# Kernel tuning notes

Measured on AMD Instinct MI355X. Metric: run time of the kernel, lower is better.

The kernel has to match this reference:

```python
import jax, jax.numpy as jnp
import numpy as np

N_EMBD = 768
N_HEAD = 12
HEAD_DIM = N_EMBD // N_HEAD


def setup_inputs() -> dict:
    key = jax.random.key(0)
    ks = jax.random.split(key, 9)
    s = 0.02
    return {
        "x": jax.random.normal(ks[0], (2, 4096, N_EMBD), dtype=jnp.float32),
        "Wq": jax.random.normal(ks[1], (N_EMBD, N_EMBD), dtype=jnp.float32) * s,
        "bq": jnp.zeros((N_EMBD,), dtype=jnp.float32),
        "Wk": jax.random.normal(ks[2], (N_EMBD, N_EMBD), dtype=jnp.float32) * s,
        "bk": jnp.zeros((N_EMBD,), dtype=jnp.float32),
        "Wv": jax.random.normal(ks[3], (N_EMBD, N_EMBD), dtype=jnp.float32) * s,
        "bv": jnp.zeros((N_EMBD,), dtype=jnp.float32),
        "Wo": jax.random.normal(ks[4], (N_EMBD, N_EMBD), dtype=jnp.float32) * s,
        "bo": jnp.zeros((N_EMBD,), dtype=jnp.float32),
    }


def reference(x, Wq, bq, Wk, bk, Wv, bv, Wo, bo):
    B, T, C = x.shape
    H, D = N_HEAD, HEAD_DIM
    # torch Linear: y = x @ W.T + b
    q = (x @ Wq.T + bq).reshape(B, T, H, D).transpose(0, 2, 1, 3)  # [B,H,T,D]
    k = (x @ Wk.T + bk).reshape(B, T, H, D).transpose(0, 2, 1, 3)
    v = (x @ Wv.T + bv).reshape(B, T, H, D).transpose(0, 2, 1, 3)
    scale = 1.0 / jnp.sqrt(jnp.float32(D))
    att = jnp.einsum("bhqd,bhkd->bhqk", q, k) * scale  # [B,H,T,T]
    causal = jnp.tril(jnp.ones((T, T), dtype=bool))
    att = jnp.where(causal[None, None], att, -jnp.inf)
    att = jax.nn.softmax(att, axis=-1)
    y = jnp.einsum("bhqk,bhkd->bhqd", att, v)
    y = y.transpose(0, 2, 1, 3).reshape(B, T, C)
    return y @ Wo.T + bo
```

## Files before the change

kernel.cpp:

```cpp
#include <hip/hip_runtime.h>

typedef __bf16 bf16_t;
typedef __bf16 bf16x4 __attribute__((ext_vector_type(4)));
typedef __bf16 bf16x8 __attribute__((ext_vector_type(8)));
typedef float  f32x4  __attribute__((ext_vector_type(4)));
typedef float  f32x16 __attribute__((ext_vector_type(16)));
typedef unsigned int u32;

#define MFMA16(a, b, c) __builtin_amdgcn_mfma_f32_16x16x32_bf16((a), (b), (c), 0, 0, 0)
#define MFMA32(a, b, c) __builtin_amdgcn_mfma_f32_32x32x16_bf16((a), (b), (c), 0, 0, 0)

__device__ __forceinline__ void gld_lds16(const bf16_t* g, bf16_t* l) {
  __builtin_amdgcn_global_load_lds((__attribute__((address_space(1))) void*)g,
                                   (__attribute__((address_space(3))) void*)l, 16, 0, 0);
}
__device__ __forceinline__ u32 cvt_pk_bf16(float lo, float hi) {
  u32 r;
  asm("v_cvt_pk_bf16_f32 %0, %1, %2" : "=v"(r) : "v"(lo), "v"(hi));
  return r;
}

__global__ void cast_f32_bf16(const float* __restrict__ s, bf16_t* __restrict__ d, int n) {
  int i = (blockIdx.x * blockDim.x + threadIdx.x) * 4;
  if (i >= n) return;
  float4 v = *(const float4*)(s + i);
  bf16x4 o;
  o[0] = (bf16_t)v.x; o[1] = (bf16_t)v.y; o[2] = (bf16_t)v.z; o[3] = (bf16_t)v.w;
  *(bf16x4*)(d + i) = o;
}

__global__ void concat_bias(const float* __restrict__ a, const float* __restrict__ b,
                            const float* __restrict__ c, float* __restrict__ d) {
  int i = blockIdx.x * blockDim.x + threadIdx.x;
  if (i >= 2304) return;
  d[i] = i < 768 ? a[i] : (i < 1536 ? b[i - 768] : c[i - 1536]);
}

__global__ __launch_bounds__(256) void gemm_qkv(
    const bf16_t* __restrict__ A, const bf16_t* __restrict__ B,
    const float* __restrict__ bias,
    bf16_t* __restrict__ qb, bf16_t* __restrict__ kb2, bf16_t* __restrict__ vtb) {
  __shared__ __align__(16) bf16_t As[128 * 64];
  __shared__ __align__(16) bf16_t Bs[128 * 64];
  const int K = 768;
  const int bm = blockIdx.x, bn = blockIdx.y;
  const int tid = threadIdx.x;
  const int w = tid >> 6, l = tid & 63, lg = l >> 4, ln = l & 15;
  const int wr = w >> 1, wc = w & 1;
  const int lr8 = l >> 3, lc8 = (l & 7) * 8;
  f32x4 acc[4][4] = {};
  for (int kb = 0; kb < K / 64; ++kb) {
    const int k0 = kb * 64;
#pragma unroll
    for (int i = 0; i < 4; ++i) {
      const int row = w * 32 + i * 8;
      gld_lds16(A + (size_t)(bm * 128 + row + lr8) * K + k0 + lc8, As + row * 64);
      gld_lds16(B + (size_t)(bn * 128 + row + lr8) * K + k0 + lc8, Bs + row * 64);
    }
    __syncthreads();
#pragma unroll
    for (int kk = 0; kk < 2; ++kk) {
      bf16x8 af[4], bfr[4];
#pragma unroll
      for (int m = 0; m < 4; ++m)
        af[m] = *(const bf16x8*)(As + (wr * 64 + m * 16 + ln) * 64 + kk * 32 + lg * 8);
#pragma unroll
      for (int n = 0; n < 4; ++n)
        bfr[n] = *(const bf16x8*)(Bs + (wc * 64 + n * 16 + ln) * 64 + kk * 32 + lg * 8);
#pragma unroll
      for (int m = 0; m < 4; ++m)
#pragma unroll
        for (int n = 0; n < 4; ++n) acc[m][n] = MFMA16(af[m], bfr[n], acc[m][n]);
    }
    __syncthreads();
  }
  const int region = (bn * 128) / 768;
  const float scl = (region == 0) ? 0.18033688011112042f : 1.0f;
  const int cbase = bn * 128 - region * 768 + wc * 64;
  const int gn0 = bn * 128 + wc * 64;
#pragma unroll
  for (int m = 0; m < 4; ++m) {
#pragma unroll
    for (int n = 0; n < 4; ++n) {
#pragma unroll
      for (int j = 0; j < 4; ++j) {
        const int gm = bm * 128 + wr * 64 + m * 16 + lg * 4 + j;
        const int gn = gn0 + n * 16 + ln;
        const float v = (acc[m][n][j] + bias[gn]) * scl;
        const int c = cbase + n * 16 + ln;
        const int bb = gm >> 12, tt = gm & 4095;
        const int hh = c >> 6, d = c & 63;
        const bf16_t bv = (bf16_t)v;
        if (region == 0)      qb [((size_t)(bb * 12 + hh) * 4096 + tt) * 64 + d] = bv;
        else if (region == 1) kb2[((size_t)(bb * 12 + hh) * 4096 + tt) * 64 + d] = bv;
        else                  vtb[((size_t)(bb * 12 + hh) * 64 + d) * 4096 + tt] = bv;
      }
    }
  }
}

__global__ __launch_bounds__(512) void attn_fwd(
    const bf16_t* __restrict__ q, const bf16_t* __restrict__ k,
    const bf16_t* __restrict__ vt, bf16_t* __restrict__ y) {
  __shared__ __align__(16) unsigned char SMEM[65536];
  bf16_t* Ks = (bf16_t*)SMEM;
  bf16_t* Vs = (bf16_t*)(SMEM + 32768);
  float*  osh = (float*)SMEM;
  float*  lsh = (float*)(SMEM + 32768);

  const int p = blockIdx.x;
  const int xcd = p & 7, slot = p >> 3;
  const int hb = xcd + 8 * (slot % 3);
  const int qt = 31 - slot / 3;
  const int tid = threadIdx.x;
  const int w = tid >> 6, l = tid & 63, lq = l & 31, lh = l >> 5;
  const int wq = w >> 1, wc = w & 1;
  const size_t hbo = (size_t)hb * (4096 * 64);
  const bf16_t* qh = q + hbo;
  const bf16_t* kh = k + hbo;
  const bf16_t* vh = vt + hbo;

  const int q0 = qt * 128 + wq * 32;
  const int qidx = q0 + lq;
  const int nst = qt + 1;

  const int sr = ((tid >> 8) << 5) | (tid & 31);
  const int sc = ((((tid >> 6) & 3) << 1) | ((tid >> 5) & 1)) << 3;
  const bf16_t* k0src = kh + ((size_t)sr * 64 + sc);
  const bf16_t* k1src = k0src + 4096;
  const bf16_t* v0src = vh + ((size_t)sr * 4096 + sc);
  const bf16_t* v1src = v0src + 64;

  bf16x8 qf[4];
#pragma unroll
  for (int ds = 0; ds < 4; ++ds)
    qf[ds] = *(const bf16x8*)(qh + (size_t)qidx * 64 + 16 * ds + 8 * lh);

  gld_lds16(k0src, Ks + tid * 8);
  gld_lds16(k1src, Ks + 4096 + tid * 8);
  gld_lds16(v0src, Vs + tid * 8);
  gld_lds16(v1src, Vs + 4096 + tid * 8);
  __syncthreads();

  f32x16 o0 = {}, o1 = {};
  float lsum = 0.f;

  int cur = 0;
  for (int i = 0; i < nst; ++i) {
    if (i + 1 < nst) {
      bf16_t* kd = Ks + (cur ^ 1) * 8192;
      bf16_t* vd = Vs + (cur ^ 1) * 8192;
      gld_lds16(k0src + 8192, kd + tid * 8);
      gld_lds16(k1src + 8192, kd + 4096 + tid * 8);
      gld_lds16(v0src + 128, vd + tid * 8);
      gld_lds16(v1src + 128, vd + 4096 + tid * 8);
    }
    k0src += 8192; k1src += 8192; v0src += 128; v1src += 128;
    const int t = 2 * i + wc;
    if (t * 64 <= q0 + 31) {
      const int kvb = t * 64;
      const bool diag = (kvb + 63 > q0);
      const bf16_t* KsW = Ks + (cur * 2 + wc) * 4096;
      const bf16_t* VsW = Vs + (cur * 2 + wc) * 4096;
      u32 pq[2][8];
#pragma unroll
      for (int kb = 0; kb < 2; ++kb) {
        f32x16 st = {};
#pragma unroll
        for (int ds = 0; ds < 4; ++ds) {
          bf16x8 kf = *(const bf16x8*)(KsW + (kb * 4 + ds) * 512 + l * 8);
          st = MFMA32(kf, qf[ds], st);
        }
        float pv[16];
#pragma unroll
        for (int r = 0; r < 16; ++r) pv[r] = __builtin_amdgcn_exp2f(st[r]);
        if (diag) {
          const int kb0 = kvb + kb * 32 + 4 * lh;
#pragma unroll
          for (int r = 0; r < 16; ++r)
            if (kb0 + (r & 3) + 8 * (r >> 2) > qidx) pv[r] = 0.f;
        }
#pragma unroll
        for (int r = 0; r < 16; ++r) lsum += pv[r];
#pragma unroll
        for (int g = 0; g < 8; ++g) pq[kb][g] = cvt_pk_bf16(pv[2 * g], pv[2 * g + 1]);
#pragma unroll
        for (int ks2 = 0; ks2 < 2; ++ks2) {
          asm("v_permlane32_swap_b32 %0, %1" : "+v"(pq[kb][4 * ks2 + 0]), "+v"(pq[kb][4 * ks2 + 2]));
          asm("v_permlane32_swap_b32 %0, %1" : "+v"(pq[kb][4 * ks2 + 1]), "+v"(pq[kb][4 * ks2 + 3]));
        }
      }
#pragma unroll
      for (int ks = 0; ks < 4; ++ks) {
        bf16x8 pa = *(const bf16x8*)&pq[ks >> 1][(ks & 1) * 4];
        bf16x8 v0 = *(const bf16x8*)(VsW + ks * 512 + l * 8);
        bf16x8 v1 = *(const bf16x8*)(VsW + (4 + ks) * 512 + l * 8);
        o0 = MFMA32(pa, v0, o0);
        o1 = MFMA32(pa, v1, o1);
      }
    }
    __syncthreads();
    cur ^= 1;
  }
  lsum += __shfl_xor(lsum, 32);

  if (wc == 1) {
#pragma unroll
    for (int r = 0; r < 16; ++r) {
      osh[wq * 2048 + r * 64 + l] = o0[r];
      osh[wq * 2048 + (16 + r) * 64 + l] = o1[r];
    }
    lsh[wq * 64 + l] = lsum;
  }
  __syncthreads();
  if (wc == 0) {
    lsum += lsh[wq * 64 + l];
#pragma unroll
    for (int r = 0; r < 16; ++r) {
      o0[r] += osh[wq * 2048 + r * 64 + l];
      o1[r] += osh[wq * 2048 + (16 + r) * 64 + l];
    }
    float linv[16];
#pragma unroll
    for (int r = 0; r < 16; ++r)
      linv[r] = 1.0f / __shfl(lsum, (r & 3) + 8 * (r >> 2) + 4 * lh);
    const int b = hb / 12, h = hb - b * 12;
#pragma unroll
    for (int r = 0; r < 16; ++r) {
      const int row = q0 + (r & 3) + 8 * (r >> 2) + 4 * lh;
      bf16_t* yr = y + ((size_t)b * 4096 + row) * 768 + h * 64 + lq;
      yr[0]  = (bf16_t)(o0[r] * linv[r]);
      yr[32] = (bf16_t)(o1[r] * linv[r]);
    }
  }
}

__global__ __launch_bounds__(256) void gemm_out(
    const bf16_t* __restrict__ A, const bf16_t* __restrict__ B,
    const float* __restrict__ bias, float* __restrict__ out) {
  __shared__ __align__(16) bf16_t As[128 * 64];
  __shared__ __align__(16) bf16_t Bs[128 * 64];
  const int K = 768;
  const int bm = blockIdx.x, bn = blockIdx.y;
  const int tid = threadIdx.x;
  const int w = tid >> 6, l = tid & 63, lg = l >> 4, ln = l & 15;
  const int wr = w >> 1, wc = w & 1;
  const int lr8 = l >> 3, lc8 = (l & 7) * 8;
  f32x4 acc[4][4] = {};
  for (int kb = 0; kb < K / 64; ++kb) {
    const int k0 = kb * 64;
#pragma unroll
    for (int i = 0; i < 4; ++i) {
      const int row = w * 32 + i * 8;
      gld_lds16(A + (size_t)(bm * 128 + row + lr8) * K + k0 + lc8, As + row * 64);
      gld_lds16(B + (size_t)(bn * 128 + row + lr8) * K + k0 + lc8, Bs + row * 64);
    }
    __syncthreads();
#pragma unroll
    for (int kk = 0; kk < 2; ++kk) {
      bf16x8 af[4], bfr[4];
#pragma unroll
      for (int m = 0; m < 4; ++m)
        af[m] = *(const bf16x8*)(As + (wr * 64 + m * 16 + ln) * 64 + kk * 32 + lg * 8);
#pragma unroll
      for (int n = 0; n < 4; ++n)
        bfr[n] = *(const bf16x8*)(Bs + (wc * 64 + n * 16 + ln) * 64 + kk * 32 + lg * 8);
#pragma unroll
      for (int m = 0; m < 4; ++m)
#pragma unroll
        for (int n = 0; n < 4; ++n) acc[m][n] = MFMA16(af[m], bfr[n], acc[m][n]);
    }
    __syncthreads();
  }
  const int gn0 = bn * 128 + wc * 64;
#pragma unroll
  for (int m = 0; m < 4; ++m) {
#pragma unroll
    for (int n = 0; n < 4; ++n) {
#pragma unroll
      for (int j = 0; j < 4; ++j) {
        const int gm = bm * 128 + wr * 64 + m * 16 + lg * 4 + j;
        const int gn = gn0 + n * 16 + ln;
        out[(size_t)gm * 768 + gn] = acc[m][n][j] + bias[gn];
      }
    }
  }
}

extern "C" void kernel_launch(void* const* d_in, const int* in_sizes, int n_in,
                              void* d_out, int out_size, void* d_ws, size_t ws_size,
                              hipStream_t stream) {
  const float* x  = (const float*)d_in[0];
  const float* Wq = (const float*)d_in[1];
  const float* bq = (const float*)d_in[2];
  const float* Wk = (const float*)d_in[3];
  const float* bk = (const float*)d_in[4];
  const float* Wv = (const float*)d_in[5];
  const float* bv = (const float*)d_in[6];
  const float* Wo = (const float*)d_in[7];
  const float* bo = (const float*)d_in[8];
  float* out = (float*)d_out;

  const int M = 8192, C = 768, QKV = 2304;
  bf16_t* xb   = (bf16_t*)d_ws;
  bf16_t* wqkv = xb + (size_t)M * C;
  bf16_t* wob  = wqkv + (size_t)QKV * C;
  float*  qkvb = (float*)(wob + (size_t)C * C);
  bf16_t* qbuf = (bf16_t*)(qkvb + QKV);
  bf16_t* kbuf = qbuf + (size_t)M * C;
  bf16_t* vtb  = kbuf + (size_t)M * C;
  bf16_t* yb   = xb;

  cast_f32_bf16<<<6144, 256, 0, stream>>>(x, xb, M * C);
  cast_f32_bf16<<<576, 256, 0, stream>>>(Wq, wqkv, C * C);
  cast_f32_bf16<<<576, 256, 0, stream>>>(Wk, wqkv + (size_t)C * C, C * C);
  cast_f32_bf16<<<576, 256, 0, stream>>>(Wv, wqkv + (size_t)2 * C * C, C * C);
  cast_f32_bf16<<<576, 256, 0, stream>>>(Wo, wob, C * C);
  concat_bias<<<9, 256, 0, stream>>>(bq, bk, bv, qkvb);

  gemm_qkv<<<dim3(64, 18), 256, 0, stream>>>(xb, wqkv, qkvb, qbuf, kbuf, vtb);
  attn_fwd<<<768, 512, 0, stream>>>(qbuf, kbuf, vtb, yb);
  gemm_out<<<dim3(64, 6), 256, 0, stream>>>(yb, wob, bo, out);
}
```

Before: 185.9 us.

## Pre-swizzle GEMM LDS layout, fuse weight casts, transpose V epilogue, add setprio

The GEMMs now load global tiles into LDS in MFMA fragment order, so each lane reads one contiguous 16-byte chunk with a simple lane-indexed address. This aims to cut LDS bank conflicts and address arithmetic. The QKV GEMM swaps operands for the V region so the transposed V store runs along the token dimension. Five weight-cast and bias launches are merged into one prep kernel, and the attention kernel wraps its MFMA blocks in s_setprio to favour matrix issue.

```diff
diff --git a/kernel.cpp b/kernel.cpp
--- a/kernel.cpp
+++ b/kernel.cpp
@@ -29,73 +29,118 @@
   *(bf16x4*)(d + i) = o;
 }
 
-__global__ void concat_bias(const float* __restrict__ a, const float* __restrict__ b,
-                            const float* __restrict__ c, float* __restrict__ d) {
-  int i = blockIdx.x * blockDim.x + threadIdx.x;
-  if (i >= 2304) return;
-  d[i] = i < 768 ? a[i] : (i < 1536 ? b[i - 768] : c[i - 1536]);
+__global__ void prep_w(const float* __restrict__ Wq, const float* __restrict__ Wk,
+                       const float* __restrict__ Wv, const float* __restrict__ Wo,
+                       const float* __restrict__ bq, const float* __restrict__ bk,
+                       const float* __restrict__ bv,
+                       bf16_t* __restrict__ wqkv, bf16_t* __restrict__ wob,
+                       float* __restrict__ qkvb) {
+  const int NW = 768 * 768;
+  const int t = blockIdx.x * 256 + threadIdx.x;
+  const int i = t * 4;
+  if (i < 3 * NW) {
+    const float* s; int off;
+    if (i < NW)          { s = Wq; off = i; }
+    else if (i < 2 * NW) { s = Wk; off = i - NW; }
+    else                 { s = Wv; off = i - 2 * NW; }
+    float4 v = *(const float4*)(s + off);
+    bf16x4 o;
+    o[0] = (bf16_t)v.x; o[1] = (bf16_t)v.y; o[2] = (bf16_t)v.z; o[3] = (bf16_t)v.w;
+    *(bf16x4*)(wqkv + i) = o;
+  } else if (i < 4 * NW) {
+    const int off = i - 3 * NW;
+    float4 v = *(const float4*)(Wo + off);
+    bf16x4 o;
+    o[0] = (bf16_t)v.x; o[1] = (bf16_t)v.y; o[2] = (bf16_t)v.z; o[3] = (bf16_t)v.w;
+    *(bf16x4*)(wob + off) = o;
+  }
+  if (t < 2304) qkvb[t] = t < 768 ? bq[t] : (t < 1536 ? bk[t - 768] : bv[t - 1536]);
 }
 
 __global__ __launch_bounds__(256) void gemm_qkv(
     const bf16_t* __restrict__ A, const bf16_t* __restrict__ B,
     const float* __restrict__ bias,
     bf16_t* __restrict__ qb, bf16_t* __restrict__ kb2, bf16_t* __restrict__ vtb) {
-  __shared__ __align__(16) bf16_t As[128 * 64];
-  __shared__ __align__(16) bf16_t Bs[128 * 64];
+  __shared__ __align__(16) bf16_t As[8192];
+  __shared__ __align__(16) bf16_t Bs[8192];
   const int K = 768;
   const int bm = blockIdx.x, bn = blockIdx.y;
   const int tid = threadIdx.x;
   const int w = tid >> 6, l = tid & 63, lg = l >> 4, ln = l & 15;
   const int wr = w >> 1, wc = w & 1;
-  const int lr8 = l >> 3, lc8 = (l & 7) * 8;
+  const int region = (bn * 128) / 768;
+  const bf16_t* sA[4]; const bf16_t* sB[4];
+#pragma unroll
+  for (int i = 0; i < 4; ++i) {
+    const int f = i * 4 + w;
+    const int row = (f >> 3) * 64 + ((f >> 1) & 3) * 16 + (l & 15);
+    const int col = (f & 1) * 32 + (l >> 4) * 8;
+    sA[i] = A + (size_t)(bm * 128 + row) * K + col;
+    sB[i] = B + (size_t)(bn * 128 + row) * K + col;
+  }
   f32x4 acc[4][4] = {};
   for (int kb = 0; kb < K / 64; ++kb) {
-    const int k0 = kb * 64;
 #pragma unroll
     for (int i = 0; i < 4; ++i) {
-      const int row = w * 32 + i * 8;
-      gld_lds16(A + (size_t)(bm * 128 + row + lr8) * K + k0 + lc8, As + row * 64);
-      gld_lds16(B + (size_t)(bn * 128 + row + lr8) * K + k0 + lc8, Bs + row * 64);
+      gld_lds16(sA[i], As + (i * 256 + w * 64) * 8);
+      gld_lds16(sB[i], Bs + (i * 256 + w * 64) * 8);
+      sA[i] += 64; sB[i] += 64;
     }
     __syncthreads();
 #pragma unroll
     for (int kk = 0; kk < 2; ++kk) {
       bf16x8 af[4], bfr[4];
 #pragma unroll
-      for (int m = 0; m < 4; ++m)
-        af[m] = *(const bf16x8*)(As + (wr * 64 + m * 16 + ln) * 64 + kk * 32 + lg * 8);
+      for (int m = 0; m < 4; ++m) {
+        af[m]  = *(const bf16x8*)(As + (wr * 8 + m * 2 + kk) * 512 + l * 8);
+        bfr[m] = *(const bf16x8*)(Bs + (wc * 8 + m * 2 + kk) * 512 + l * 8);
+      }
+      if (region != 2) {
+#pragma unroll
+        for (int m = 0; m < 4; ++m)
+#pragma unroll
+          for (int n = 0; n < 4; ++n) acc[m][n] = MFMA16(af[m], bfr[n], acc[m][n]);
+      } else {
+#pragma unroll
+        for (int m = 0; m < 4; ++m)
+#pragma unroll
+          for (int n = 0; n < 4; ++n) acc[m][n] = MFMA16(bfr[n], af[m], acc[m][n]);
+      }
+    }
+    __syncthreads();
+  }
+  if (region != 2) {
+    const float scl = (region == 0) ? 0.18033688011112042f : 1.0f;
+    bf16_t* dst = region == 0 ? qb : kb2;
+#pragma unroll
+    for (int m = 0; m < 4; ++m)
 #pragma unroll
       for (int n = 0; n < 4; ++n)
-        bfr[n] = *(const bf16x8*)(Bs + (wc * 64 + n * 16 + ln) * 64 + kk * 32 + lg * 8);
-#pragma unroll
-      for (int m = 0; m < 4; ++m)
-#pragma unroll
-        for (int n = 0; n < 4; ++n) acc[m][n] = MFMA16(af[m], bfr[n], acc[m][n]);
-    }
-    __syncthreads();
-  }
-  const int region = (bn * 128) / 768;
-  const float scl = (region == 0) ? 0.18033688011112042f : 1.0f;
-  const int cbase = bn * 128 - region * 768 + wc * 64;
-  const int gn0 = bn * 128 + wc * 64;
-#pragma unroll
-  for (int m = 0; m < 4; ++m) {
-#pragma unroll
-    for (int n = 0; n < 4; ++n) {
-#pragma unroll
-      for (int j = 0; j < 4; ++j) {
-        const int gm = bm * 128 + wr * 64 + m * 16 + lg * 4 + j;
-        const int gn = gn0 + n * 16 + ln;
-        const float v = (acc[m][n][j] + bias[gn]) * scl;
-        const int c = cbase + n * 16 + ln;
-        const int bb = gm >> 12, tt = gm & 4095;
-        const int hh = c >> 6, d = c & 63;
-        const bf16_t bv = (bf16_t)v;
-        if (region == 0)      qb [((size_t)(bb * 12 + hh) * 4096 + tt) * 64 + d] = bv;
-        else if (region == 1) kb2[((size_t)(bb * 12 + hh) * 4096 + tt) * 64 + d] = bv;
-        else                  vtb[((size_t)(bb * 12 + hh) * 64 + d) * 4096 + tt] = bv;
-      }
-    }
+#pragma unroll
+        for (int j = 0; j < 4; ++j) {
+          const int gm = bm * 128 + wr * 64 + m * 16 + lg * 4 + j;
+          const int gn = bn * 128 + wc * 64 + n * 16 + ln;
+          const float v = (acc[m][n][j] + bias[gn]) * scl;
+          const int c = gn - region * 768;
+          const int bb = gm >> 12, tt = gm & 4095;
+          const int hh = c >> 6, d = c & 63;
+          dst[((size_t)(bb * 12 + hh) * 4096 + tt) * 64 + d] = (bf16_t)v;
+        }
+  } else {
+#pragma unroll
+    for (int m = 0; m < 4; ++m)
+#pragma unroll
+      for (int n = 0; n < 4; ++n)
+#pragma unroll
+        for (int j = 0; j < 4; ++j) {
+          const int gn = bn * 128 + wc * 64 + n * 16 + lg * 4 + j;
+          const int gm = bm * 128 + wr * 64 + m * 16 + ln;
+          const float v = acc[m][n][j] + bias[gn];
+          const int c = gn - 1536;
+          const int bb = gm >> 12, tt = gm & 4095;
+          const int hh = c >> 6, d = c & 63;
+          vtb[((size_t)(bb * 12 + hh) * 64 + d) * 4096 + tt] = (bf16_t)v;
+        }
   }
 }
 
@@ -166,11 +211,13 @@
 #pragma unroll
       for (int kb = 0; kb < 2; ++kb) {
         f32x16 st = {};
+        __builtin_amdgcn_s_setprio(1);
 #pragma unroll
         for (int ds = 0; ds < 4; ++ds) {
           bf16x8 kf = *(const bf16x8*)(KsW + (kb * 4 + ds) * 512 + l * 8);
           st = MFMA32(kf, qf[ds], st);
         }
+        __builtin_amdgcn_s_setprio(0);
         float pv[16];
 #pragma unroll
         for (int r = 0; r < 16; ++r) pv[r] = __builtin_amdgcn_exp2f(st[r]);
@@ -190,6 +237,7 @@
           asm("v_permlane32_swap_b32 %0, %1" : "+v"(pq[kb][4 * ks2 + 1]), "+v"(pq[kb][4 * ks2 + 3]));
         }
       }
+      __builtin_amdgcn_s_setprio(1);
 #pragma unroll
       for (int ks = 0; ks < 4; ++ks) {
         bf16x8 pa = *(const bf16x8*)&pq[ks >> 1][(ks & 1) * 4];
@@ -198,6 +246,7 @@
         o0 = MFMA32(pa, v0, o0);
         o1 = MFMA32(pa, v1, o1);
       }
+      __builtin_amdgcn_s_setprio(0);
     }
     __syncthreads();
     cur ^= 1;
@@ -238,33 +287,39 @@
 __global__ __launch_bounds__(256) void gemm_out(
     const bf16_t* __restrict__ A, const bf16_t* __restrict__ B,
     const float* __restrict__ bias, float* __restrict__ out) {
-  __shared__ __align__(16) bf16_t As[128 * 64];
-  __shared__ __align__(16) bf16_t Bs[128 * 64];
+  __shared__ __align__(16) bf16_t As[8192];
+  __shared__ __align__(16) bf16_t Bs[8192];
   const int K = 768;
   const int bm = blockIdx.x, bn = blockIdx.y;
   const int tid = threadIdx.x;
   const int w = tid >> 6, l = tid & 63, lg = l >> 4, ln = l & 15;
   const int wr = w >> 1, wc = w & 1;
-  const int lr8 = l >> 3, lc8 = (l & 7) * 8;
+  const bf16_t* sA[4]; const bf16_t* sB[4];
+#pragma unroll
+  for (int i = 0; i < 4; ++i) {
+    const int f = i * 4 + w;
+    const int row = (f >> 3) * 64 + ((f >> 1) & 3) * 16 + (l & 15);
+    const int col = (f & 1) * 32 + (l >> 4) * 8;
+    sA[i] = A + (size_t)(bm * 128 + row) * K + col;
+    sB[i] = B + (size_t)(bn * 128 + row) * K + col;
+  }
   f32x4 acc[4][4] = {};
   for (int kb = 0; kb < K / 64; ++kb) {
-    const int k0 = kb * 64;
 #pragma unroll
     for (int i = 0; i < 4; ++i) {
-      const int row = w * 32 + i * 8;
-      gld_lds16(A + (size_t)(bm * 128 + row + lr8) * K + k0 + lc8, As + row * 64);
-      gld_lds16(B + (size_t)(bn * 128 + row + lr8) * K + k0 + lc8, Bs + row * 64);
+      gld_lds16(sA[i], As + (i * 256 + w * 64) * 8);
+      gld_lds16(sB[i], Bs + (i * 256 + w * 64) * 8);
+      sA[i] += 64; sB[i] += 64;
     }
     __syncthreads();
 #pragma unroll
     for (int kk = 0; kk < 2; ++kk) {
       bf16x8 af[4], bfr[4];
 #pragma unroll
-      for (int m = 0; m < 4; ++m)
-        af[m] = *(const bf16x8*)(As + (wr * 64 + m * 16 + ln) * 64 + kk * 32 + lg * 8);
-#pragma unroll
-      for (int n = 0; n < 4; ++n)
-        bfr[n] = *(const bf16x8*)(Bs + (wc * 64 + n * 16 + ln) * 64 + kk * 32 + lg * 8);
+      for (int m = 0; m < 4; ++m) {
+        af[m]  = *(const bf16x8*)(As + (wr * 8 + m * 2 + kk) * 512 + l * 8);
+        bfr[m] = *(const bf16x8*)(Bs + (wc * 8 + m * 2 + kk) * 512 + l * 8);
+      }
 #pragma unroll
       for (int m = 0; m < 4; ++m)
 #pragma unroll
@@ -312,11 +367,7 @@
   bf16_t* yb   = xb;
 
   cast_f32_bf16<<<6144, 256, 0, stream>>>(x, xb, M * C);
-  cast_f32_bf16<<<576, 256, 0, stream>>>(Wq, wqkv, C * C);
-  cast_f32_bf16<<<576, 256, 0, stream>>>(Wk, wqkv + (size_t)C * C, C * C);
-  cast_f32_bf16<<<576, 256, 0, stream>>>(Wv, wqkv + (size_t)2 * C * C, C * C);
-  cast_f32_bf16<<<576, 256, 0, stream>>>(Wo, wob, C * C);
-  concat_bias<<<9, 256, 0, stream>>>(bq, bk, bv, qkvb);
+  prep_w<<<2304, 256, 0, stream>>>(Wq, Wk, Wv, Wo, bq, bk, bv, wqkv, wob, qkvb);
 
   gemm_qkv<<<dim3(64, 18), 256, 0, stream>>>(xb, wqkv, qkvb, qbuf, kbuf, vtb);
   attn_fwd<<<768, 512, 0, stream>>>(qbuf, kbuf, vtb, yb);
```

After: 214.1 us. 1.15x slower.
